# Kernel optimization log

Hardware: AMD Instinct MI355X
Metric: run time of the kernel (lower is better)

The kernel has to match this reference:

```python
import jax, jax.numpy as jnp
import numpy as np

# static configuration (matches init_kwargs)
CTX = 512   # context_dim
D = 512     # d_model
H = 8       # nhead
HD = D // H
L = 4       # num_layers
FF = 2048   # dim_feedforward
P = 24      # prediction_length
TS = 1      # time_series_dim
B = 256     # batch size
NEG = -1e9  # additive mask value (== -inf after softmax in fp32)


def _pos_encoding():
    pos = np.arange(P, dtype=np.float32)[:, None]
    div = np.exp(np.arange(0, D, 2, dtype=np.float32) * (-np.log(10000.0) / D))
    pe = np.zeros((P, D), dtype=np.float32)
    pe[:, 0::2] = np.sin(pos * div)
    pe[:, 1::2] = np.cos(pos * div)
    return jnp.asarray(pe[:, None, :])  # [P, 1, D] (seq-first broadcast over batch)


def setup_inputs() -> dict:
    key = jax.random.key(0)
    ks = iter(jax.random.split(key, 64))
    def g(shape, scale=0.02):
        return jax.random.normal(next(ks), shape, dtype=jnp.float32) * scale
    return {
        "context": jax.random.normal(next(ks), (B, CTX), dtype=jnp.float32),
        "start_token": g((1, 1, TS), 1.0),
        "ctx_W": g((D, CTX)), "ctx_b": jnp.zeros((D,), jnp.float32),
        "ve_W": g((D, TS)),   "ve_b": jnp.zeros((D,), jnp.float32),
        "sa_in_w": g((L, 3 * D, D)), "sa_in_b": jnp.zeros((L, 3 * D), jnp.float32),
        "sa_out_w": g((L, D, D)),    "sa_out_b": jnp.zeros((L, D), jnp.float32),
        "ca_in_w": g((L, 3 * D, D)), "ca_in_b": jnp.zeros((L, 3 * D), jnp.float32),
        "ca_out_w": g((L, D, D)),    "ca_out_b": jnp.zeros((L, D), jnp.float32),
        "lin1_w": g((L, FF, D)), "lin1_b": jnp.zeros((L, FF), jnp.float32),
        "lin2_w": g((L, D, FF)), "lin2_b": jnp.zeros((L, D), jnp.float32),
        "ln1_w": jnp.ones((L, D), jnp.float32), "ln1_b": jnp.zeros((L, D), jnp.float32),
        "ln2_w": jnp.ones((L, D), jnp.float32), "ln2_b": jnp.zeros((L, D), jnp.float32),
        "ln3_w": jnp.ones((L, D), jnp.float32), "ln3_b": jnp.zeros((L, D), jnp.float32),
        "o1_w": g((D // 2, D)), "o1_b": jnp.zeros((D // 2,), jnp.float32),
        "o2_w": g((TS, D // 2)), "o2_b": jnp.zeros((TS,), jnp.float32),
    }


def _layer_norm(x, w, b, eps=1e-5):
    m = jnp.mean(x, -1, keepdims=True)
    v = jnp.mean(jnp.square(x - m), -1, keepdims=True)
    return (x - m) / jnp.sqrt(v + eps) * w + b


def _mha(q_in, kv_in, in_w, in_b, out_w, out_b, mask):
    # q_in: [S,B,D] seq-first, kv_in: [T,B,D]
    Wq, Wk, Wv = jnp.split(in_w, 3, axis=0)
    bq, bk, bv = jnp.split(in_b, 3)
    S = q_in.shape[0]; T = kv_in.shape[0]
    q = (q_in @ Wq.T + bq).reshape(S, -1, H, HD)
    k = (kv_in @ Wk.T + bk).reshape(T, -1, H, HD)
    v = (kv_in @ Wv.T + bv).reshape(T, -1, H, HD)
    scores = jnp.einsum('sbhd,tbhd->bhst', q, k) / np.sqrt(HD).astype(np.float32)
    if mask is not None:
        scores = scores + mask
    attn = jax.nn.softmax(scores, axis=-1)
    o = jnp.einsum('bhst,tbhd->sbhd', attn, v).reshape(S, -1, D)
    return o @ out_w.T + out_b


def reference(context, start_token, ctx_W, ctx_b, ve_W, ve_b,
              sa_in_w, sa_in_b, sa_out_w, sa_out_b,
              ca_in_w, ca_in_b, ca_out_w, ca_out_b,
              lin1_w, lin1_b, lin2_w, lin2_b,
              ln1_w, ln1_b, ln2_w, ln2_b, ln3_w, ln3_b,
              o1_w, o1_b, o2_w, o2_b):
    pe = _pos_encoding()
    causal = jnp.where(jnp.tril(jnp.ones((P, P), bool)), 0.0, NEG)[None, None]  # [1,1,P,P]
    memory = (context @ ctx_W.T + ctx_b)[None]  # [1,B,D]

    def decode(vals):
        # vals: [P+1,B,TS]; only the first P slots form the (padded) target sequence.
        # Causal mask guarantees position t only sees slots <= t, so reading
        # position t reproduces the original length-(t+1) decode exactly.
        x = vals[:P] @ ve_W.T + ve_b + pe  # [P,B,D]
        for i in range(L):
            sa = _mha(x, x, sa_in_w[i], sa_in_b[i], sa_out_w[i], sa_out_b[i], causal)
            x = _layer_norm(x + sa, ln1_w[i], ln1_b[i])
            ca = _mha(x, memory, ca_in_w[i], ca_in_b[i], ca_out_w[i], ca_out_b[i], None)
            x = _layer_norm(x + ca, ln2_w[i], ln2_b[i])
            h = jax.nn.gelu(x @ lin1_w[i].T + lin1_b[i], approximate=False)
            x = _layer_norm(x + h @ lin2_w[i].T + lin2_b[i], ln3_w[i], ln3_b[i])
        return x

    def step(vals, t):
        x = decode(vals)
        last = jnp.take(x, t, axis=0)  # [B,D] output at current last position
        h = jax.nn.gelu(last @ o1_w.T + o1_b, approximate=False)
        nv = h @ o2_w.T + o2_b  # [B,TS]
        vals = jax.lax.dynamic_update_slice(vals, nv[None], (t + 1, 0, 0))
        return vals, nv

    vals0 = jnp.zeros((P + 1, B, TS), jnp.float32)
    vals0 = vals0.at[0].set(jnp.broadcast_to(start_token[0, 0], (B, TS)))
    _, ys = jax.lax.scan(jax.checkpoint(step), vals0, jnp.arange(P))
    return jnp.transpose(ys, (1, 0, 2))  # [B,P,TS]
```

## Files before the change

kernel.cpp:

```cpp
#include <hip/hip_runtime.h>
#include <math.h>


#define B    256
#define D    512
#define H    8
#define HD   64
#define L    4
#define FF   2048
#define P    24
#define NBLK 256
#define NTHR 512
#define NGRP 8
#define GSZ  32
#define CS   ((size_t)B * H * P * HD)

typedef float f4 __attribute__((ext_vector_type(4)));
typedef float f2 __attribute__((ext_vector_type(2)));

struct MegaArgs {
  const float *context, *start_token, *ctx_W, *ctx_b, *ve_W, *ve_b;
  const float *sa_in_w, *sa_in_b, *sa_out_w, *sa_out_b;
  const float *ca_in_w, *ca_in_b, *ca_out_w, *ca_out_b;
  const float *lin1_w, *lin1_b, *lin2_w, *lin2_b;
  const float *ln1_w, *ln1_b, *ln2_w, *ln2_b, *ln3_w, *ln3_b;
  const float *o1_w, *o1_b, *o2_w, *o2_b;
  float *out;
  float *pe, *vals, *memory, *ca_add, *x, *qbuf, *hbuf, *part, *hh,
        *kcache, *vcache;
};

__device__ __forceinline__ float gld(const float* p)
{
  return __hip_atomic_load((float*)p, __ATOMIC_RELAXED,
                           __HIP_MEMORY_SCOPE_AGENT);
}
__device__ __forceinline__ void gst(float* p, float v)
{
  __hip_atomic_store(p, v, __ATOMIC_RELAXED, __HIP_MEMORY_SCOPE_AGENT);
}
__device__ __forceinline__ void gst4(float* p, f4 v)
{
  asm volatile("global_store_dwordx4 %0, %1, off sc0 sc1"
               :: "v"(p), "v"(v) : "memory");
}
__device__ __forceinline__ f4 gld4e(const float* p)
{
  f4 r;
  asm volatile("global_load_dwordx4 %0, %1, off sc0 sc1\n\t"
               "s_waitcnt vmcnt(0)"
               : "=&v"(r) : "v"(p) : "memory");
  return r;
}

__device__ __align__(128) unsigned g_cnt[NGRP * 32];
__device__ __align__(128) unsigned g_root = 0;
__device__ __align__(128) unsigned g_gen  = 0;
__device__ __align__(128) unsigned g_base = 0;

__device__ __forceinline__ void grid_bar(unsigned &bno)
{
  ++bno;
  asm volatile("s_waitcnt vmcnt(0)" ::: "memory");
  __syncthreads();
  if (threadIdx.x == 0) {
    unsigned* cnt = &g_cnt[(blockIdx.x & (NGRP - 1)) * 32];
    const unsigned o = __hip_atomic_fetch_add(cnt, 1u, __ATOMIC_RELAXED,
                                              __HIP_MEMORY_SCOPE_AGENT);
    if (o == bno * GSZ - 1u) {
      const unsigned r = __hip_atomic_fetch_add(&g_root, 1u, __ATOMIC_RELAXED,
                                                __HIP_MEMORY_SCOPE_AGENT);
      if (r == bno * NGRP - 1u)
        __hip_atomic_store(&g_gen, bno, __ATOMIC_RELAXED,
                           __HIP_MEMORY_SCOPE_AGENT);
    }
    while (__hip_atomic_load(&g_gen, __ATOMIC_RELAXED,
                             __HIP_MEMORY_SCOPE_AGENT) < bno)
      __builtin_amdgcn_s_sleep(2);
  }
  __syncthreads();
}

__device__ __forceinline__ float gelu_f(float v)
{
  return 0.5f * v * (1.0f + erff(v * 0.70710678118654752f));
}
__device__ __forceinline__ f4 gelu4(f4 v)
{
  v.x = gelu_f(v.x); v.y = gelu_f(v.y); v.z = gelu_f(v.z); v.w = gelu_f(v.w);
  return v;
}

template <int LOADER, int EPI>
__device__ void gemmK(float* sh,
                      const float* A, int lda,
                      const float* W, int ldw, const float* bias,
                      float* C, int ldc, int m0, int n0, int k0, int KL,
                      float* kcp, float* vcp, int t,
                      const float* valst, const float* veW, const float* veb,
                      const float* pet)
{
  float* As = sh;
  float* Ws = sh + 16 * 68;
  const int tid = threadIdx.x;
  const int tm = tid >> 4;
  const int tn = tid & 15;
  float acc[2][4] = {};

  float vv0 = 0.f, vv1 = 0.f;
  if constexpr (LOADER == 1) {
    vv0 = valst[m0 + (tid >> 4)];
    vv1 = valst[m0 + 32 + (tid >> 4)];
  }

  for (int kb = 0; kb < KL; kb += 16) {
#pragma unroll
    for (int i = 0; i < 2; i++) {
      const int idx = tid + i * 512;
      const int r = idx >> 4;
      const int c = idx & 15;
      const int k = k0 + kb + c;
      float av;
      if constexpr (LOADER == 1) {
        av = (i ? vv1 : vv0) * veW[k] + veb[k] + pet[k];
      } else if constexpr (LOADER == 2) {
        av = A[(size_t)(m0 + r) * lda + k];
      } else {
        av = gld(A + (size_t)(m0 + r) * lda + k);
      }
      As[c * 68 + r] = av;
      Ws[c * 68 + r] = W[(size_t)(n0 + r) * ldw + k];
    }
    __syncthreads();
#pragma unroll
    for (int kk = 0; kk < 16; kk++) {
      const f2 a2 = *(const f2*)(As + kk * 68 + tm * 2);
      const f4 w4 = *(const f4*)(Ws + kk * 68 + tn * 4);
      acc[0][0] = fmaf(a2.x, w4.x, acc[0][0]);
      acc[0][1] = fmaf(a2.x, w4.y, acc[0][1]);
      acc[0][2] = fmaf(a2.x, w4.z, acc[0][2]);
      acc[0][3] = fmaf(a2.x, w4.w, acc[0][3]);
      acc[1][0] = fmaf(a2.y, w4.x, acc[1][0]);
      acc[1][1] = fmaf(a2.y, w4.y, acc[1][1]);
      acc[1][2] = fmaf(a2.y, w4.z, acc[1][2]);
      acc[1][3] = fmaf(a2.y, w4.w, acc[1][3]);
    }
    __syncthreads();
  }

  const int n4 = n0 + tn * 4;
#pragma unroll
  for (int i = 0; i < 2; i++) {
    const int m = m0 + tm * 2 + i;
    f4 v;
    v.x = acc[i][0]; v.y = acc[i][1]; v.z = acc[i][2]; v.w = acc[i][3];
    if constexpr (EPI != 3) v += *(const f4*)(bias + n4);
    if constexpr (EPI == 1) v = gelu4(v);
    if constexpr (EPI == 2) {
      if (n4 < D) {
        gst4(C + (size_t)m * D + n4, v);
      } else if (n4 < 2 * D) {
        const int f = n4 - D;
        gst4(kcp + ((size_t)(m * H + (f >> 6)) * P + t) * HD + (f & 63), v);
      } else {
        const int f = n4 - 2 * D;
        gst4(vcp + ((size_t)(m * H + (f >> 6)) * P + t) * HD + (f & 63), v);
      }
    } else {
      gst4(C + (size_t)m * ldc + n4, v);
    }
  }
}

__device__ __forceinline__ float rsum128(float v, float* sb)
{
#pragma unroll
  for (int o = 32; o; o >>= 1) v += __shfl_xor(v, o);
  const int w = threadIdx.x >> 6;
  if ((threadIdx.x & 63) == 0) sb[w] = v;
  __syncthreads();
  const int rl = threadIdx.x >> 7;
  const float s = sb[rl * 2] + sb[rl * 2 + 1];
  __syncthreads();
  return s;
}

#define NKMAP(b) ((((b) >> 5) << 3) | ((b) & 7))
#define MMAP(b)  (((b) >> 3) & 3)

__global__ __launch_bounds__(NTHR) void mega(MegaArgs a)
{
  __shared__ float sh[2 * 16 * 68];
  __shared__ float sbf[8];
  const int blk = blockIdx.x;
  unsigned bno = __hip_atomic_load(&g_base, __ATOMIC_RELAXED,
                                   __HIP_MEMORY_SCOPE_AGENT);
  float* attn_o = a.part + (size_t)4 * B * D;

  if (blk < 32) {
    gemmK<2, 0>(sh, a.context, 512, a.ctx_W, 512, a.ctx_b, a.memory, D,
                (blk & 3) * 64, (blk >> 2) * 64, 0, 512,
                nullptr, nullptr, 0, nullptr, nullptr, nullptr, nullptr);
  } else if (blk < 56) {
    const int tt = blk - 32;
    const int dd = threadIdx.x;
    const float fr = expf((float)(dd & ~1) * (-9.210340371976184f / (float)D));
    const float ang = (float)tt * fr;
    gst(a.pe + tt * D + dd, (dd & 1) ? cosf(ang) : sinf(ang));
  } else if (blk == 56) {
    if (threadIdx.x < B) gst(a.vals + threadIdx.x, a.start_token[0]);
  }
  grid_bar(bno);

  if (blk < 128) {
    const int l = blk >> 5, tile = blk & 31;
    gemmK<2, 0>(sh, a.memory, D,
                a.ca_in_w + (size_t)l * 3 * D * D + (size_t)2 * D * D, D,
                a.ca_in_b + l * 3 * D + 2 * D,
                a.part + (size_t)l * B * D, D,
                (tile & 3) * 64, (tile >> 2) * 64, 0, 512,
                nullptr, nullptr, 0, nullptr, nullptr, nullptr, nullptr);
  }
  grid_bar(bno);

  if (blk < 128) {
    const int l = blk >> 5, tile = blk & 31;
    gemmK<2, 0>(sh, a.part + (size_t)l * B * D, D,
                a.ca_out_w + (size_t)l * D * D, D, a.ca_out_b + l * D,
                a.ca_add + (size_t)l * B * D, D,
                (tile & 3) * 64, (tile >> 2) * 64, 0, 512,
                nullptr, nullptr, 0, nullptr, nullptr, nullptr, nullptr);
  }
  grid_bar(bno);

  for (int t = 0; t < P; t++) {
    for (int l = 0; l < L; l++) {
      float* kcp = a.kcache + (size_t)l * CS;
      float* vcp = a.vcache + (size_t)l * CS;

      if (blk < 96) {
        const int m0 = MMAP(blk) * 64, n0 = NKMAP(blk) * 64;
        if (l == 0)
          gemmK<1, 2>(sh, nullptr, 0, a.sa_in_w, D, a.sa_in_b, a.qbuf, D,
                      m0, n0, 0, 512, kcp, vcp, t,
                      a.vals + (size_t)t * B, a.ve_W, a.ve_b,
                      a.pe + (size_t)t * D);
        else
          gemmK<0, 2>(sh, a.x, D, a.sa_in_w + (size_t)l * 3 * D * D, D,
                      a.sa_in_b + l * 3 * D, a.qbuf, D, m0, n0, 0, 512,
                      kcp, vcp, t, nullptr, nullptr, nullptr, nullptr);
      }
      grid_bar(bno);

      {
        const int wid = threadIdx.x >> 6, lane = threadIdx.x & 63;
        const int u = blk * 8 + wid;
        const int b = u >> 3, h = u & 7;
        const int g = lane >> 4;
        const int hd0 = (lane & 15) * 4;
        const float* kb = kcp + (size_t)(b * H + h) * P * HD;
        const float* vb = vcp + (size_t)(b * H + h) * P * HD;
        const f4 q4 = gld4e(a.qbuf + (size_t)b * D + h * HD + hd0);
        const int nn = t + 1;
        float p[6];
#pragma unroll
        for (int bt = 0; bt < 6; bt++) {
          const int j = bt * 4 + g;
          float s = -1e30f;
          if (j < nn) {
            const f4 k4 = *(const f4*)(kb + j * HD + hd0);
            s = q4.x * k4.x + q4.y * k4.y + q4.z * k4.z + q4.w * k4.w;
          }
#pragma unroll
          for (int o = 1; o <= 8; o <<= 1) s += __shfl_xor(s, o);
          p[bt] = s * 0.125f;
        }
        float mx = -1e30f;
#pragma unroll
        for (int bt = 0; bt < 6; bt++)
          if (bt * 4 + g < nn) mx = fmaxf(mx, p[bt]);
        mx = fmaxf(mx, __shfl_xor(mx, 16));
        mx = fmaxf(mx, __shfl_xor(mx, 32));
        float sum = 0.f;
#pragma unroll
        for (int bt = 0; bt < 6; bt++) {
          const int j = bt * 4 + g;
          const float e = (j < nn) ? expf(p[bt] - mx) : 0.f;
          p[bt] = e; sum += e;
        }
        sum += __shfl_xor(sum, 16);
        sum += __shfl_xor(sum, 32);
        const float inv = 1.0f / sum;
        f4 o4 = {0.f, 0.f, 0.f, 0.f};
#pragma unroll
        for (int j = 0; j < P; j++)
          if (j < nn) {
            const float pj = __shfl(p[j >> 2], ((j & 3) << 4) | (lane & 15));
            const f4 v4 = *(const f4*)(vb + j * HD + hd0);
            o4 += (pj * inv) * v4;
          }
        gst4(attn_o + (size_t)b * D + h * HD + hd0, o4);
      }
      grid_bar(bno);

      if (blk < 128) {
        const int nk = NKMAP(blk);
        gemmK<0, 3>(sh, attn_o, D, a.sa_out_w + (size_t)l * D * D, D,
                    nullptr, a.part + (size_t)(nk >> 3) * B * D, D,
                    MMAP(blk) * 64, (nk & 7) * 64, (nk >> 3) * 128, 128,
                    nullptr, nullptr, 0, nullptr, nullptr, nullptr, nullptr);
      }
      grid_bar(bno);

      if (blk < 64) {
        const int row = blk * 4 + (threadIdx.x >> 7);
        const int cc = (threadIdx.x & 127) * 4;
        const size_t o = (size_t)row * D + cc;
        f4 u;
        if (l == 0) {
          const float vv = a.vals[(size_t)t * B + row];
          u = vv * (*(const f4*)(a.ve_W + cc)) + *(const f4*)(a.ve_b + cc)
              + *(const f4*)(a.pe + (size_t)t * D + cc);
        } else {
          u = gld4e(a.x + o);
        }
        u += *(const f4*)(a.sa_out_b + l * D + cc);
        u += gld4e(a.part + o);
        u += gld4e(a.part + (size_t)B * D + o);
        u += gld4e(a.part + (size_t)2 * B * D + o);
        u += gld4e(a.part + (size_t)3 * B * D + o);
        const float m1 = rsum128(u.x + u.y + u.z + u.w, sbf) * (1.0f / D);
        f4 d = u - m1;
        const float v1 =
            rsum128(d.x * d.x + d.y * d.y + d.z * d.z + d.w * d.w, sbf)
            * (1.0f / D);
        f4 z = d * rsqrtf(v1 + 1e-5f) * (*(const f4*)(a.ln1_w + l * D + cc))
               + *(const f4*)(a.ln1_b + l * D + cc);
        f4 r2 = z + *(const f4*)(a.ca_add + (size_t)l * B * D + o);
        const float m2 = rsum128(r2.x + r2.y + r2.z + r2.w, sbf) * (1.0f / D);
        f4 d2 = r2 - m2;
        const float v2 =
            rsum128(d2.x * d2.x + d2.y * d2.y + d2.z * d2.z + d2.w * d2.w,
                    sbf) * (1.0f / D);
        f4 z2 = d2 * rsqrtf(v2 + 1e-5f) * (*(const f4*)(a.ln2_w + l * D + cc))
                + *(const f4*)(a.ln2_b + l * D + cc);
        gst4(a.x + o, z2);
      }
      grid_bar(bno);

      if (blk < 128)
        gemmK<0, 1>(sh, a.x, D, a.lin1_w + (size_t)l * FF * D, D,
                    a.lin1_b + l * FF, a.hbuf, FF,
                    MMAP(blk) * 64, NKMAP(blk) * 64, 0, 512,
                    nullptr, nullptr, 0, nullptr, nullptr, nullptr, nullptr);
      grid_bar(bno);

      {
        const int nk = NKMAP(blk);
        gemmK<0, 3>(sh, a.hbuf, FF, a.lin2_w + (size_t)l * D * FF, FF,
                    nullptr, a.part + (size_t)(nk >> 3) * B * D, D,
                    MMAP(blk) * 64, (nk & 7) * 64, (nk >> 3) * 256, 256,
                    nullptr, nullptr, 0, nullptr, nullptr, nullptr, nullptr);
      }
      grid_bar(bno);

      if (blk < 64) {
        const int row = blk * 4 + (threadIdx.x >> 7);
        const int cc = (threadIdx.x & 127) * 4;
        const size_t o = (size_t)row * D + cc;
        f4 s0 = gld4e(a.x + o) + *(const f4*)(a.lin2_b + l * D + cc);
#pragma unroll
        for (int kc = 0; kc < 8; kc++)
          s0 += gld4e(a.part + (size_t)kc * B * D + o);
        const float m1 = rsum128(s0.x + s0.y + s0.z + s0.w, sbf) * (1.0f / D);
        f4 d = s0 - m1;
        const float v1 =
            rsum128(d.x * d.x + d.y * d.y + d.z * d.z + d.w * d.w, sbf)
            * (1.0f / D);
        f4 z = d * rsqrtf(v1 + 1e-5f) * (*(const f4*)(a.ln3_w + l * D + cc))
               + *(const f4*)(a.ln3_b + l * D + cc);
        gst4(a.x + o, z);
      }
      grid_bar(bno);
    }

    if (blk < 16)
      gemmK<0, 1>(sh, a.x, D, a.o1_w, D, a.o1_b, a.hh, 256,
                  (blk & 3) * 64, (blk >> 2) * 64, 0, 512,
                  nullptr, nullptr, 0, nullptr, nullptr, nullptr, nullptr);
    grid_bar(bno);

    if (blk < 32) {
      const int wid = threadIdx.x >> 6, lane = threadIdx.x & 63;
      const int r = blk * 8 + wid;
      const f4 hv = gld4e(a.hh + (size_t)r * 256 + lane * 4);
      const f4 wv = *(const f4*)(a.o2_w + lane * 4);
      float pp = hv.x * wv.x + hv.y * wv.y + hv.z * wv.z + hv.w * wv.w;
#pragma unroll
      for (int o = 32; o; o >>= 1) pp += __shfl_xor(pp, o);
      if (lane == 0) {
        const float v = pp + a.o2_b[0];
        gst(a.vals + (size_t)(t + 1) * B + r, v);
        a.out[(size_t)r * P + t] = v;
      }
    }
    grid_bar(bno);
  }

  if (blk == 0 && threadIdx.x == 0)
    __hip_atomic_store(&g_base, bno, __ATOMIC_RELAXED,
                       __HIP_MEMORY_SCOPE_AGENT);
}

extern "C" void kernel_launch(void* const* d_in, const int* in_sizes, int n_in,
                              void* d_out, int out_size, void* d_ws,
                              size_t ws_size, hipStream_t stream)
{
  (void)in_sizes; (void)n_in; (void)out_size; (void)ws_size;
  MegaArgs h;
  h.context     = (const float*)d_in[0];
  h.start_token = (const float*)d_in[1];
  h.ctx_W  = (const float*)d_in[2];
  h.ctx_b  = (const float*)d_in[3];
  h.ve_W   = (const float*)d_in[4];
  h.ve_b   = (const float*)d_in[5];
  h.sa_in_w  = (const float*)d_in[6];
  h.sa_in_b  = (const float*)d_in[7];
  h.sa_out_w = (const float*)d_in[8];
  h.sa_out_b = (const float*)d_in[9];
  h.ca_in_w  = (const float*)d_in[10];
  h.ca_in_b  = (const float*)d_in[11];
  h.ca_out_w = (const float*)d_in[12];
  h.ca_out_b = (const float*)d_in[13];
  h.lin1_w = (const float*)d_in[14];
  h.lin1_b = (const float*)d_in[15];
  h.lin2_w = (const float*)d_in[16];
  h.lin2_b = (const float*)d_in[17];
  h.ln1_w = (const float*)d_in[18];
  h.ln1_b = (const float*)d_in[19];
  h.ln2_w = (const float*)d_in[20];
  h.ln2_b = (const float*)d_in[21];
  h.ln3_w = (const float*)d_in[22];
  h.ln3_b = (const float*)d_in[23];
  h.o1_w = (const float*)d_in[24];
  h.o1_b = (const float*)d_in[25];
  h.o2_w = (const float*)d_in[26];
  h.o2_b = (const float*)d_in[27];
  h.out = (float*)d_out;

  float* ws = (float*)d_ws;
  size_t off = 0;
  h.pe      = ws + off; off += (size_t)P * D;
  h.vals    = ws + off; off += (size_t)(P + 1) * B;
  h.memory  = ws + off; off += (size_t)B * D;
  h.ca_add  = ws + off; off += (size_t)L * B * D;
  h.x       = ws + off; off += (size_t)B * D;
  h.qbuf    = ws + off; off += (size_t)B * D;
  h.hbuf    = ws + off; off += (size_t)B * FF;
  h.part    = ws + off; off += (size_t)8 * B * D;
  h.hh      = ws + off; off += (size_t)B * 256;
  h.kcache  = ws + off; off += (size_t)L * CS;
  h.vcache  = ws + off; off += (size_t)L * CS;

  void* kargs[] = { &h };
  hipLaunchCooperativeKernel(mega, dim3(NBLK), dim3(NTHR), kargs, 0, stream);
}
```

Before: 12.78 ms.

## Fuse per-row attention, out-proj and layernorms into one stage; double-buffer GEMM tiles

Restructures the decoder step so each block owns one batch row. That block scatters K/V into the cache, runs attention, does the self-attention output projection and the LN1/cross-attn/LN2 work in-block, and also runs the o1/o2 head. This removes several grid barriers per layer. The QKV GEMM now uses split-K over 192 blocks with the bias added during the fused stage. The shared GEMM is double-buffered with a 32-wide K chunk and prefetches the next tile, and the grid barrier spins on per-group generation flags. The trade-off is redundant per-row weight reads (sa_out_w, o1_w read by every block) in exchange for fewer synchronizations.

```diff
diff --git a/kernel.cpp b/kernel.cpp
--- a/kernel.cpp
+++ b/kernel.cpp
@@ -3,6 +3,7 @@
 
 
 #define B    256
+#define CTX  512
 #define D    512
 #define H    8
 #define HD   64
@@ -26,8 +27,7 @@
   const float *ln1_w, *ln1_b, *ln2_w, *ln2_b, *ln3_w, *ln3_b;
   const float *o1_w, *o1_b, *o2_w, *o2_b;
   float *out;
-  float *pe, *vals, *memory, *ca_add, *x, *qbuf, *hbuf, *part, *hh,
-        *kcache, *vcache;
+  float *pe, *vals, *ca_add, *x, *part, *hbuf, *kcache, *vcache;
 };
 
 __device__ __forceinline__ float gld(const float* p)
@@ -39,6 +39,17 @@
 {
   __hip_atomic_store(p, v, __ATOMIC_RELAXED, __HIP_MEMORY_SCOPE_AGENT);
 }
+#define GLD4(dst, ptr) \
+  asm volatile("global_load_dwordx4 %0, %1, off sc0 sc1" \
+               : "=&v"(dst) : "v"(ptr))
+#define GLD1(dst, ptr) \
+  asm volatile("global_load_dword %0, %1, off sc0 sc1" \
+               : "=&v"(dst) : "v"(ptr))
+__device__ __forceinline__ void gwait()
+{
+  asm volatile("s_waitcnt vmcnt(0)" ::: "memory");
+  __builtin_amdgcn_sched_barrier(0);
+}
 __device__ __forceinline__ void gst4(float* p, f4 v)
 {
   asm volatile("global_store_dwordx4 %0, %1, off sc0 sc1"
@@ -47,15 +58,14 @@
 __device__ __forceinline__ f4 gld4e(const float* p)
 {
   f4 r;
-  asm volatile("global_load_dwordx4 %0, %1, off sc0 sc1\n\t"
-               "s_waitcnt vmcnt(0)"
-               : "=&v"(r) : "v"(p) : "memory");
+  GLD4(r, p);
+  gwait();
   return r;
 }
 
 __device__ __align__(128) unsigned g_cnt[NGRP * 32];
 __device__ __align__(128) unsigned g_root = 0;
-__device__ __align__(128) unsigned g_gen  = 0;
+__device__ __align__(128) unsigned g_gen[NGRP * 32];
 __device__ __align__(128) unsigned g_base = 0;
 
 __device__ __forceinline__ void grid_bar(unsigned &bno)
@@ -64,19 +74,25 @@
   asm volatile("s_waitcnt vmcnt(0)" ::: "memory");
   __syncthreads();
   if (threadIdx.x == 0) {
-    unsigned* cnt = &g_cnt[(blockIdx.x & (NGRP - 1)) * 32];
-    const unsigned o = __hip_atomic_fetch_add(cnt, 1u, __ATOMIC_RELAXED,
-                                              __HIP_MEMORY_SCOPE_AGENT);
+    const int grp = blockIdx.x & (NGRP - 1);
+    const unsigned o = __hip_atomic_fetch_add(&g_cnt[grp * 32], 1u,
+                         __ATOMIC_RELAXED, __HIP_MEMORY_SCOPE_AGENT);
     if (o == bno * GSZ - 1u) {
-      const unsigned r = __hip_atomic_fetch_add(&g_root, 1u, __ATOMIC_RELAXED,
-                                                __HIP_MEMORY_SCOPE_AGENT);
-      if (r == bno * NGRP - 1u)
-        __hip_atomic_store(&g_gen, bno, __ATOMIC_RELAXED,
-                           __HIP_MEMORY_SCOPE_AGENT);
+      const unsigned r = __hip_atomic_fetch_add(&g_root, 1u,
+                           __ATOMIC_RELAXED, __HIP_MEMORY_SCOPE_AGENT);
+      if (r == bno * NGRP - 1u) {
+#pragma unroll
+        for (int g = 0; g < NGRP; g++)
+          __hip_atomic_store(&g_gen[g * 32], bno, __ATOMIC_RELAXED,
+                             __HIP_MEMORY_SCOPE_AGENT);
+      }
     }
-    while (__hip_atomic_load(&g_gen, __ATOMIC_RELAXED,
-                             __HIP_MEMORY_SCOPE_AGENT) < bno)
-      __builtin_amdgcn_s_sleep(2);
+    if (__hip_atomic_load(&g_gen[grp * 32], __ATOMIC_RELAXED,
+                          __HIP_MEMORY_SCOPE_AGENT) < bno) {
+      do { __builtin_amdgcn_s_sleep(16); }
+      while (__hip_atomic_load(&g_gen[grp * 32], __ATOMIC_RELAXED,
+                               __HIP_MEMORY_SCOPE_AGENT) < bno);
+    }
   }
   __syncthreads();
 }
@@ -92,50 +108,57 @@
 }
 
 template <int LOADER, int EPI>
-__device__ void gemmK(float* sh,
+__device__ void gemmK(float* shmem,
                       const float* A, int lda,
                       const float* W, int ldw, const float* bias,
                       float* C, int ldc, int m0, int n0, int k0, int KL,
-                      float* kcp, float* vcp, int t,
                       const float* valst, const float* veW, const float* veb,
                       const float* pet)
 {
-  float* As = sh;
-  float* Ws = sh + 16 * 68;
   const int tid = threadIdx.x;
+  const int r  = tid >> 3;
+  const int kl = (tid & 7) * 4;
   const int tm = tid >> 4;
   const int tn = tid & 15;
+
+  float vsc = 0.f;
+  if constexpr (LOADER == 1) vsc = valst[m0 + r];
+
+  f4 va, vw;
+  auto issue = [&](int kb) {
+    const int k = k0 + kb + kl;
+    if constexpr (LOADER == 1) {
+      va = vsc * (*(const f4*)(veW + k)) + (*(const f4*)(veb + k))
+           + (*(const f4*)(pet + k));
+    } else if constexpr (LOADER == 2) {
+      va = *(const f4*)(A + (size_t)(m0 + r) * lda + k);
+    } else {
+      GLD4(va, A + (size_t)(m0 + r) * lda + k);
+    }
+    vw = *(const f4*)(W + (size_t)(n0 + r) * ldw + k);
+  };
+
+  issue(0);
   float acc[2][4] = {};
-
-  float vv0 = 0.f, vv1 = 0.f;
-  if constexpr (LOADER == 1) {
-    vv0 = valst[m0 + (tid >> 4)];
-    vv1 = valst[m0 + 32 + (tid >> 4)];
-  }
-
-  for (int kb = 0; kb < KL; kb += 16) {
-#pragma unroll
-    for (int i = 0; i < 2; i++) {
-      const int idx = tid + i * 512;
-      const int r = idx >> 4;
-      const int c = idx & 15;
-      const int k = k0 + kb + c;
-      float av;
-      if constexpr (LOADER == 1) {
-        av = (i ? vv1 : vv0) * veW[k] + veb[k] + pet[k];
-      } else if constexpr (LOADER == 2) {
-        av = A[(size_t)(m0 + r) * lda + k];
-      } else {
-        av = gld(A + (size_t)(m0 + r) * lda + k);
-      }
-      As[c * 68 + r] = av;
-      Ws[c * 68 + r] = W[(size_t)(n0 + r) * ldw + k];
-    }
+  const int nch = KL / 32;
+  for (int ch = 0; ch < nch; ch++) {
+    float* as = shmem + (ch & 1) * (2 * 32 * 68);
+    float* ws = as + 32 * 68;
+    if constexpr (LOADER == 0) gwait();
+    as[(kl + 0) * 68 + r] = va.x;
+    as[(kl + 1) * 68 + r] = va.y;
+    as[(kl + 2) * 68 + r] = va.z;
+    as[(kl + 3) * 68 + r] = va.w;
+    ws[(kl + 0) * 68 + r] = vw.x;
+    ws[(kl + 1) * 68 + r] = vw.y;
+    ws[(kl + 2) * 68 + r] = vw.z;
+    ws[(kl + 3) * 68 + r] = vw.w;
     __syncthreads();
-#pragma unroll
-    for (int kk = 0; kk < 16; kk++) {
-      const f2 a2 = *(const f2*)(As + kk * 68 + tm * 2);
-      const f4 w4 = *(const f4*)(Ws + kk * 68 + tn * 4);
+    if (ch + 1 < nch) issue((ch + 1) * 32);
+#pragma unroll
+    for (int kk = 0; kk < 32; kk++) {
+      const f2 a2 = *(const f2*)(as + kk * 68 + tm * 2);
+      const f4 w4 = *(const f4*)(ws + kk * 68 + tn * 4);
       acc[0][0] = fmaf(a2.x, w4.x, acc[0][0]);
       acc[0][1] = fmaf(a2.x, w4.y, acc[0][1]);
       acc[0][2] = fmaf(a2.x, w4.z, acc[0][2]);
@@ -152,84 +175,74 @@
 #pragma unroll
   for (int i = 0; i < 2; i++) {
     const int m = m0 + tm * 2 + i;
-    f4 v;
-    v.x = acc[i][0]; v.y = acc[i][1]; v.z = acc[i][2]; v.w = acc[i][3];
+    f4 v = {acc[i][0], acc[i][1], acc[i][2], acc[i][3]};
     if constexpr (EPI != 3) v += *(const f4*)(bias + n4);
     if constexpr (EPI == 1) v = gelu4(v);
-    if constexpr (EPI == 2) {
-      if (n4 < D) {
-        gst4(C + (size_t)m * D + n4, v);
-      } else if (n4 < 2 * D) {
-        const int f = n4 - D;
-        gst4(kcp + ((size_t)(m * H + (f >> 6)) * P + t) * HD + (f & 63), v);
-      } else {
-        const int f = n4 - 2 * D;
-        gst4(vcp + ((size_t)(m * H + (f >> 6)) * P + t) * HD + (f & 63), v);
-      }
-    } else {
-      gst4(C + (size_t)m * ldc + n4, v);
-    }
-  }
-}
-
-__device__ __forceinline__ float rsum128(float v, float* sb)
+    gst4(C + (size_t)m * ldc + n4, v);
+  }
+}
+
+__device__ __forceinline__ float rsum512(float v, float* sbf)
 {
 #pragma unroll
   for (int o = 32; o; o >>= 1) v += __shfl_xor(v, o);
-  const int w = threadIdx.x >> 6;
-  if ((threadIdx.x & 63) == 0) sb[w] = v;
+  const int wid = threadIdx.x >> 6;
+  if ((threadIdx.x & 63) == 0) sbf[wid] = v;
   __syncthreads();
-  const int rl = threadIdx.x >> 7;
-  const float s = sb[rl * 2] + sb[rl * 2 + 1];
+  float s = 0.f;
+#pragma unroll
+  for (int w = 0; w < 8; w++) s += sbf[w];
   __syncthreads();
   return s;
 }
 
-#define NKMAP(b) ((((b) >> 5) << 3) | ((b) & 7))
-#define MMAP(b)  (((b) >> 3) & 3)
-
 __global__ __launch_bounds__(NTHR) void mega(MegaArgs a)
 {
-  __shared__ float sh[2 * 16 * 68];
+  __shared__ float sh[4 * 32 * 68];
+  __shared__ float rowbuf[1536];
+  __shared__ float attn_s[512];
   __shared__ float sbf[8];
   const int blk = blockIdx.x;
+  const int tid = threadIdx.x;
   unsigned bno = __hip_atomic_load(&g_base, __ATOMIC_RELAXED,
                                    __HIP_MEMORY_SCOPE_AGENT);
-  float* attn_o = a.part + (size_t)4 * B * D;
+
+  float* qkvA = a.part;
+  float* qkvB = a.part + (size_t)B * 1536;
+  float* memory = a.hbuf;
 
   if (blk < 32) {
-    gemmK<2, 0>(sh, a.context, 512, a.ctx_W, 512, a.ctx_b, a.memory, D,
+    gemmK<2, 0>(sh, a.context, CTX, a.ctx_W, CTX, a.ctx_b, memory, D,
                 (blk & 3) * 64, (blk >> 2) * 64, 0, 512,
-                nullptr, nullptr, 0, nullptr, nullptr, nullptr, nullptr);
+                nullptr, nullptr, nullptr, nullptr);
   } else if (blk < 56) {
     const int tt = blk - 32;
-    const int dd = threadIdx.x;
-    const float fr = expf((float)(dd & ~1) * (-9.210340371976184f / (float)D));
+    const float fr = expf((float)(tid & ~1) * (-9.210340371976184f / (float)D));
     const float ang = (float)tt * fr;
-    gst(a.pe + tt * D + dd, (dd & 1) ? cosf(ang) : sinf(ang));
+    gst(a.pe + tt * D + tid, (tid & 1) ? cosf(ang) : sinf(ang));
   } else if (blk == 56) {
-    if (threadIdx.x < B) gst(a.vals + threadIdx.x, a.start_token[0]);
+    if (tid < B) gst(a.vals + tid, a.start_token[0]);
   }
   grid_bar(bno);
 
   if (blk < 128) {
     const int l = blk >> 5, tile = blk & 31;
-    gemmK<2, 0>(sh, a.memory, D,
+    gemmK<0, 0>(sh, memory, D,
                 a.ca_in_w + (size_t)l * 3 * D * D + (size_t)2 * D * D, D,
                 a.ca_in_b + l * 3 * D + 2 * D,
                 a.part + (size_t)l * B * D, D,
                 (tile & 3) * 64, (tile >> 2) * 64, 0, 512,
-                nullptr, nullptr, 0, nullptr, nullptr, nullptr, nullptr);
+                nullptr, nullptr, nullptr, nullptr);
   }
   grid_bar(bno);
 
   if (blk < 128) {
     const int l = blk >> 5, tile = blk & 31;
-    gemmK<2, 0>(sh, a.part + (size_t)l * B * D, D,
+    gemmK<0, 0>(sh, a.part + (size_t)l * B * D, D,
                 a.ca_out_w + (size_t)l * D * D, D, a.ca_out_b + l * D,
                 a.ca_add + (size_t)l * B * D, D,
                 (tile & 3) * 64, (tile >> 2) * 64, 0, 512,
-                nullptr, nullptr, 0, nullptr, nullptr, nullptr, nullptr);
+                nullptr, nullptr, nullptr, nullptr);
   }
   grid_bar(bno);
 
@@ -238,176 +251,238 @@
       float* kcp = a.kcache + (size_t)l * CS;
       float* vcp = a.vcache + (size_t)l * CS;
 
-      if (blk < 96) {
-        const int m0 = MMAP(blk) * 64, n0 = NKMAP(blk) * 64;
+      if (blk < 192) {
+        const int wq = (blk >> 5) * 8 + (blk & 7);
+        const int m = (blk >> 3) & 3;
+        const int nt = wq >> 1, kc = wq & 1;
+        float* dst = kc ? qkvB : qkvA;
         if (l == 0)
-          gemmK<1, 2>(sh, nullptr, 0, a.sa_in_w, D, a.sa_in_b, a.qbuf, D,
-                      m0, n0, 0, 512, kcp, vcp, t,
+          gemmK<1, 3>(sh, nullptr, 0, a.sa_in_w, D, nullptr,
+                      dst, 1536, m * 64, nt * 64, kc * 256, 256,
                       a.vals + (size_t)t * B, a.ve_W, a.ve_b,
                       a.pe + (size_t)t * D);
         else
-          gemmK<0, 2>(sh, a.x, D, a.sa_in_w + (size_t)l * 3 * D * D, D,
-                      a.sa_in_b + l * 3 * D, a.qbuf, D, m0, n0, 0, 512,
-                      kcp, vcp, t, nullptr, nullptr, nullptr, nullptr);
+          gemmK<0, 3>(sh, a.x, D, a.sa_in_w + (size_t)l * 3 * D * D, D,
+                      nullptr, dst, 1536, m * 64, nt * 64, kc * 256, 256,
+                      nullptr, nullptr, nullptr, nullptr);
       }
       grid_bar(bno);
 
       {
-        const int wid = threadIdx.x >> 6, lane = threadIdx.x & 63;
-        const int u = blk * 8 + wid;
-        const int b = u >> 3, h = u & 7;
-        const int g = lane >> 4;
-        const int hd0 = (lane & 15) * 4;
-        const float* kb = kcp + (size_t)(b * H + h) * P * HD;
-        const float* vb = vcp + (size_t)(b * H + h) * P * HD;
-        const f4 q4 = gld4e(a.qbuf + (size_t)b * D + h * HD + hd0);
-        const int nn = t + 1;
-        float p[6];
-#pragma unroll
-        for (int bt = 0; bt < 6; bt++) {
-          const int j = bt * 4 + g;
-          float s = -1e30f;
-          if (j < nn) {
-            const f4 k4 = *(const f4*)(kb + j * HD + hd0);
-            s = q4.x * k4.x + q4.y * k4.y + q4.z * k4.z + q4.w * k4.w;
+        const int b = blk;
+        if (tid < 384) {
+          f4 pa, pb;
+          GLD4(pa, qkvA + (size_t)b * 1536 + tid * 4);
+          GLD4(pb, qkvB + (size_t)b * 1536 + tid * 4);
+          gwait();
+          f4 s = pa + pb + *(const f4*)(a.sa_in_b + l * 3 * D + tid * 4);
+          *(f4*)(rowbuf + tid * 4) = s;
+        }
+        __syncthreads();
+        if (tid < 256) {
+          const int half = tid >> 7;
+          const int d = (tid & 127) * 4;
+          const int h = d >> 6, hd = d & 63;
+          f4 kv = *(const f4*)(rowbuf + 512 + half * 512 + d);
+          float* cp = (half ? vcp : kcp)
+                      + ((size_t)(b * H + h) * P + t) * HD + hd;
+          gst4(cp, kv);
+        }
+        __syncthreads();
+        {
+          const int h = tid >> 6, lane = tid & 63;
+          const int g = lane >> 4, hd0 = (lane & 15) * 4;
+          const float* kb = kcp + (size_t)(b * H + h) * P * HD;
+          const float* vb = vcp + (size_t)(b * H + h) * P * HD;
+          const f4 q4 = *(const f4*)(rowbuf + h * HD + hd0);
+          const int nn = t + 1;
+          float pp[6];
+#pragma unroll
+          for (int bt = 0; bt < 6; bt++) {
+            const int j = bt * 4 + g;
+            float s = -1e30f;
+            if (j < nn) {
+              const f4 k4 = *(const f4*)(kb + j * HD + hd0);
+              s = q4.x * k4.x + q4.y * k4.y + q4.z * k4.z + q4.w * k4.w;
+            }
+#pragma unroll
+            for (int o = 1; o <= 8; o <<= 1) s += __shfl_xor(s, o);
+            pp[bt] = s * 0.125f;
           }
-#pragma unroll
-          for (int o = 1; o <= 8; o <<= 1) s += __shfl_xor(s, o);
-          p[bt] = s * 0.125f;
+          float mx = -1e30f;
+#pragma unroll
+          for (int bt = 0; bt < 6; bt++)
+            if (bt * 4 + g < nn) mx = fmaxf(mx, pp[bt]);
+          mx = fmaxf(mx, __shfl_xor(mx, 16));
+          mx = fmaxf(mx, __shfl_xor(mx, 32));
+          float sum = 0.f;
+#pragma unroll
+          for (int bt = 0; bt < 6; bt++) {
+            const int j = bt * 4 + g;
+            const float e = (j < nn) ? expf(pp[bt] - mx) : 0.f;
+            pp[bt] = e; sum += e;
+          }
+          sum += __shfl_xor(sum, 16);
+          sum += __shfl_xor(sum, 32);
+          const float inv = 1.0f / sum;
+          f4 o4 = {0.f, 0.f, 0.f, 0.f};
+#pragma unroll
+          for (int j = 0; j < P; j++)
+            if (j < nn) {
+              const float pj = __shfl(pp[j >> 2], ((j & 3) << 4) | (lane & 15));
+              const f4 v4 = *(const f4*)(vb + j * HD + hd0);
+              o4 += pj * v4;
+            }
+          o4 *= inv;
+          *(f4*)(attn_s + h * HD + hd0) = o4;
         }
-        float mx = -1e30f;
-#pragma unroll
-        for (int bt = 0; bt < 6; bt++)
-          if (bt * 4 + g < nn) mx = fmaxf(mx, p[bt]);
-        mx = fmaxf(mx, __shfl_xor(mx, 16));
-        mx = fmaxf(mx, __shfl_xor(mx, 32));
-        float sum = 0.f;
-#pragma unroll
-        for (int bt = 0; bt < 6; bt++) {
-          const int j = bt * 4 + g;
-          const float e = (j < nn) ? expf(p[bt] - mx) : 0.f;
-          p[bt] = e; sum += e;
+        __syncthreads();
+        {
+          const int n = tid;
+          const float* wrow = a.sa_out_w + (size_t)l * D * D + (size_t)n * D;
+          float xres;
+          if (l == 0) {
+            const float vv = a.vals[(size_t)t * B + b];
+            xres = vv * a.ve_W[n] + a.ve_b[n] + a.pe[(size_t)t * D + n];
+          } else {
+            xres = gld(a.x + (size_t)b * D + n);
+          }
+          float ac0 = 0.f, ac1 = 0.f, ac2 = 0.f, ac3 = 0.f;
+#pragma unroll 4
+          for (int k = 0; k < D; k += 16) {
+            const f4 w0 = *(const f4*)(wrow + k);
+            const f4 w1 = *(const f4*)(wrow + k + 4);
+            const f4 w2 = *(const f4*)(wrow + k + 8);
+            const f4 w3 = *(const f4*)(wrow + k + 12);
+            const f4 x0 = *(const f4*)(attn_s + k);
+            const f4 x1 = *(const f4*)(attn_s + k + 4);
+            const f4 x2 = *(const f4*)(attn_s + k + 8);
+            const f4 x3 = *(const f4*)(attn_s + k + 12);
+            ac0 = fmaf(w0.x, x0.x, ac0); ac0 = fmaf(w0.y, x0.y, ac0);
+            ac0 = fmaf(w0.z, x0.z, ac0); ac0 = fmaf(w0.w, x0.w, ac0);
+            ac1 = fmaf(w1.x, x1.x, ac1); ac1 = fmaf(w1.y, x1.y, ac1);
+            ac1 = fmaf(w1.z, x1.z, ac1); ac1 = fmaf(w1.w, x1.w, ac1);
+            ac2 = fmaf(w2.x, x2.x, ac2); ac2 = fmaf(w2.y, x2.y, ac2);
+            ac2 = fmaf(w2.z, x2.z, ac2); ac2 = fmaf(w2.w, x2.w, ac2);
+            ac3 = fmaf(w3.x, x3.x, ac3); ac3 = fmaf(w3.y, x3.y, ac3);
+            ac3 = fmaf(w3.z, x3.z, ac3); ac3 = fmaf(w3.w, x3.w, ac3);
+          }
+          float u = xres + (ac0 + ac1) + (ac2 + ac3) + a.sa_out_b[l * D + n];
+          const float m1 = rsum512(u, sbf) * (1.0f / D);
+          const float d1 = u - m1;
+          const float v1 = rsum512(d1 * d1, sbf) * (1.0f / D);
+          float z = d1 * rsqrtf(v1 + 1e-5f) * a.ln1_w[l * D + n]
+                    + a.ln1_b[l * D + n];
+          z += a.ca_add[(size_t)l * B * D + (size_t)b * D + n];
+          const float m2 = rsum512(z, sbf) * (1.0f / D);
+          const float d2 = z - m2;
+          const float v2 = rsum512(d2 * d2, sbf) * (1.0f / D);
+          rowbuf[n] = d2 * rsqrtf(v2 + 1e-5f) * a.ln2_w[l * D + n]
+                      + a.ln2_b[l * D + n];
         }
-        sum += __shfl_xor(sum, 16);
-        sum += __shfl_xor(sum, 32);
-        const float inv = 1.0f / sum;
-        f4 o4 = {0.f, 0.f, 0.f, 0.f};
-#pragma unroll
-        for (int j = 0; j < P; j++)
-          if (j < nn) {
-            const float pj = __shfl(p[j >> 2], ((j & 3) << 4) | (lane & 15));
-            const f4 v4 = *(const f4*)(vb + j * HD + hd0);
-            o4 += (pj * inv) * v4;
-          }
-        gst4(attn_o + (size_t)b * D + h * HD + hd0, o4);
+        __syncthreads();
+        if (tid < 128)
+          gst4(a.x + (size_t)blk * D + tid * 4, *(const f4*)(rowbuf + tid * 4));
       }
       grid_bar(bno);
 
       if (blk < 128) {
-        const int nk = NKMAP(blk);
-        gemmK<0, 3>(sh, attn_o, D, a.sa_out_w + (size_t)l * D * D, D,
-                    nullptr, a.part + (size_t)(nk >> 3) * B * D, D,
-                    MMAP(blk) * 64, (nk & 7) * 64, (nk >> 3) * 128, 128,
-                    nullptr, nullptr, 0, nullptr, nullptr, nullptr, nullptr);
-      }
-      grid_bar(bno);
-
-      if (blk < 64) {
-        const int row = blk * 4 + (threadIdx.x >> 7);
-        const int cc = (threadIdx.x & 127) * 4;
-        const size_t o = (size_t)row * D + cc;
-        f4 u;
-        if (l == 0) {
-          const float vv = a.vals[(size_t)t * B + row];
-          u = vv * (*(const f4*)(a.ve_W + cc)) + *(const f4*)(a.ve_b + cc)
-              + *(const f4*)(a.pe + (size_t)t * D + cc);
-        } else {
-          u = gld4e(a.x + o);
-        }
-        u += *(const f4*)(a.sa_out_b + l * D + cc);
-        u += gld4e(a.part + o);
-        u += gld4e(a.part + (size_t)B * D + o);
-        u += gld4e(a.part + (size_t)2 * B * D + o);
-        u += gld4e(a.part + (size_t)3 * B * D + o);
-        const float m1 = rsum128(u.x + u.y + u.z + u.w, sbf) * (1.0f / D);
-        f4 d = u - m1;
-        const float v1 =
-            rsum128(d.x * d.x + d.y * d.y + d.z * d.z + d.w * d.w, sbf)
-            * (1.0f / D);
-        f4 z = d * rsqrtf(v1 + 1e-5f) * (*(const f4*)(a.ln1_w + l * D + cc))
-               + *(const f4*)(a.ln1_b + l * D + cc);
-        f4 r2 = z + *(const f4*)(a.ca_add + (size_t)l * B * D + o);
-        const float m2 = rsum128(r2.x + r2.y + r2.z + r2.w, sbf) * (1.0f / D);
-        f4 d2 = r2 - m2;
-        const float v2 =
-            rsum128(d2.x * d2.x + d2.y * d2.y + d2.z * d2.z + d2.w * d2.w,
-                    sbf) * (1.0f / D);
-        f4 z2 = d2 * rsqrtf(v2 + 1e-5f) * (*(const f4*)(a.ln2_w + l * D + cc))
-                + *(const f4*)(a.ln2_b + l * D + cc);
-        gst4(a.x + o, z2);
-      }
-      grid_bar(bno);
-
-      if (blk < 128)
+        const int wt = (blk >> 5) * 8 + (blk & 7);
+        const int m = (blk >> 3) & 3;
         gemmK<0, 1>(sh, a.x, D, a.lin1_w + (size_t)l * FF * D, D,
                     a.lin1_b + l * FF, a.hbuf, FF,
-                    MMAP(blk) * 64, NKMAP(blk) * 64, 0, 512,
-                    nullptr, nullptr, 0, nullptr, nullptr, nullptr, nullptr);
+                    m * 64, wt * 64, 0, 512,
+                    nullptr, nullptr, nullptr, nullptr);
+      }
       grid_bar(bno);
 
       {
-        const int nk = NKMAP(blk);
+        const int wt = (blk >> 5) * 8 + (blk & 7);
+        const int m = (blk >> 3) & 3;
+        const int nt = wt >> 3, kc = wt & 7;
         gemmK<0, 3>(sh, a.hbuf, FF, a.lin2_w + (size_t)l * D * FF, FF,
-                    nullptr, a.part + (size_t)(nk >> 3) * B * D, D,
-                    MMAP(blk) * 64, (nk & 7) * 64, (nk >> 3) * 256, 256,
-                    nullptr, nullptr, 0, nullptr, nullptr, nullptr, nullptr);
+                    nullptr, a.part + (size_t)kc * B * D, D,
+                    m * 64, nt * 64, kc * 256, 256,
+                    nullptr, nullptr, nullptr, nullptr);
       }
       grid_bar(bno);
 
-      if (blk < 64) {
-        const int row = blk * 4 + (threadIdx.x >> 7);
-        const int cc = (threadIdx.x & 127) * 4;
-        const size_t o = (size_t)row * D + cc;
-        f4 s0 = gld4e(a.x + o) + *(const f4*)(a.lin2_b + l * D + cc);
-#pragma unroll
-        for (int kc = 0; kc < 8; kc++)
-          s0 += gld4e(a.part + (size_t)kc * B * D + o);
-        const float m1 = rsum128(s0.x + s0.y + s0.z + s0.w, sbf) * (1.0f / D);
-        f4 d = s0 - m1;
-        const float v1 =
-            rsum128(d.x * d.x + d.y * d.y + d.z * d.z + d.w * d.w, sbf)
-            * (1.0f / D);
-        f4 z = d * rsqrtf(v1 + 1e-5f) * (*(const f4*)(a.ln3_w + l * D + cc))
-               + *(const f4*)(a.ln3_b + l * D + cc);
-        gst4(a.x + o, z);
+      {
+        const int b = blk, n = tid;
+        const size_t o = (size_t)b * D + n;
+        float xv, p0, p1, p2, p3, p4, p5, p6, p7;
+        GLD1(xv, a.x + o);
+        GLD1(p0, a.part + o);
+        GLD1(p1, a.part + (size_t)1 * B * D + o);
+        GLD1(p2, a.part + (size_t)2 * B * D + o);
+        GLD1(p3, a.part + (size_t)3 * B * D + o);
+        GLD1(p4, a.part + (size_t)4 * B * D + o);
+        GLD1(p5, a.part + (size_t)5 * B * D + o);
+        GLD1(p6, a.part + (size_t)6 * B * D + o);
+        GLD1(p7, a.part + (size_t)7 * B * D + o);
+        gwait();
+        float s0 = xv + a.lin2_b[l * D + n]
+                 + ((p0 + p1) + (p2 + p3)) + ((p4 + p5) + (p6 + p7));
+        const float m1 = rsum512(s0, sbf) * (1.0f / D);
+        const float d1 = s0 - m1;
+        const float v1 = rsum512(d1 * d1, sbf) * (1.0f / D);
+        rowbuf[n] = d1 * rsqrtf(v1 + 1e-5f) * a.ln3_w[l * D + n]
+                    + a.ln3_b[l * D + n];
+        __syncthreads();
+        if (tid < 128)
+          gst4(a.x + (size_t)b * D + tid * 4, *(const f4*)(rowbuf + tid * 4));
       }
       grid_bar(bno);
     }
 
-    if (blk < 16)
-      gemmK<0, 1>(sh, a.x, D, a.o1_w, D, a.o1_b, a.hh, 256,
-                  (blk & 3) * 64, (blk >> 2) * 64, 0, 512,
-                  nullptr, nullptr, 0, nullptr, nullptr, nullptr, nullptr);
-    grid_bar(bno);
-
-    if (blk < 32) {
-      const int wid = threadIdx.x >> 6, lane = threadIdx.x & 63;
-      const int r = blk * 8 + wid;
-      const f4 hv = gld4e(a.hh + (size_t)r * 256 + lane * 4);
-      const f4 wv = *(const f4*)(a.o2_w + lane * 4);
-      float pp = hv.x * wv.x + hv.y * wv.y + hv.z * wv.z + hv.w * wv.w;
-#pragma unroll
-      for (int o = 32; o; o >>= 1) pp += __shfl_xor(pp, o);
-      if (lane == 0) {
-        const float v = pp + a.o2_b[0];
-        gst(a.vals + (size_t)(t + 1) * B + r, v);
-        a.out[(size_t)r * P + t] = v;
+    {
+      const int b = blk;
+      if (tid < 128)
+        *(f4*)(rowbuf + tid * 4) = gld4e(a.x + (size_t)b * D + tid * 4);
+      __syncthreads();
+      if (tid < 256) {
+        const float* wrow = a.o1_w + (size_t)tid * D;
+        float ac0 = 0.f, ac1 = 0.f, ac2 = 0.f, ac3 = 0.f;
+#pragma unroll 4
+        for (int k = 0; k < D; k += 16) {
+          const f4 w0 = *(const f4*)(wrow + k);
+          const f4 w1 = *(const f4*)(wrow + k + 4);
+          const f4 w2 = *(const f4*)(wrow + k + 8);
+          const f4 w3 = *(const f4*)(wrow + k + 12);
+          const f4 x0 = *(const f4*)(rowbuf + k);
+          const f4 x1 = *(const f4*)(rowbuf + k + 4);
+          const f4 x2 = *(const f4*)(rowbuf + k + 8);
+          const f4 x3 = *(const f4*)(rowbuf + k + 12);
+          ac0 = fmaf(w0.x, x0.x, ac0); ac0 = fmaf(w0.y, x0.y, ac0);
+          ac0 = fmaf(w0.z, x0.z, ac0); ac0 = fmaf(w0.w, x0.w, ac0);
+          ac1 = fmaf(w1.x, x1.x, ac1); ac1 = fmaf(w1.y, x1.y, ac1);
+          ac1 = fmaf(w1.z, x1.z, ac1); ac1 = fmaf(w1.w, x1.w, ac1);
+          ac2 = fmaf(w2.x, x2.x, ac2); ac2 = fmaf(w2.y, x2.y, ac2);
+          ac2 = fmaf(w2.z, x2.z, ac2); ac2 = fmaf(w2.w, x2.w, ac2);
+          ac3 = fmaf(w3.x, x3.x, ac3); ac3 = fmaf(w3.y, x3.y, ac3);
+          ac3 = fmaf(w3.z, x3.z, ac3); ac3 = fmaf(w3.w, x3.w, ac3);
+        }
+        attn_s[tid] = gelu_f((ac0 + ac1) + (ac2 + ac3) + a.o1_b[tid]);
+      }
+      __syncthreads();
+      if (tid < 64) {
+        float p = 0.f;
+#pragma unroll
+        for (int j = 0; j < 4; j++)
+          p = fmaf(attn_s[tid * 4 + j], a.o2_w[tid * 4 + j], p);
+#pragma unroll
+        for (int o = 32; o; o >>= 1) p += __shfl_xor(p, o);
+        if (tid == 0) {
+          const float v = p + a.o2_b[0];
+          gst(a.vals + (size_t)(t + 1) * B + b, v);
+          a.out[(size_t)b * P + t] = v;
+        }
       }
     }
     grid_bar(bno);
   }
 
-  if (blk == 0 && threadIdx.x == 0)
+  if (blk == 0 && tid == 0)
     __hip_atomic_store(&g_base, bno, __ATOMIC_RELAXED,
                        __HIP_MEMORY_SCOPE_AGENT);
 }
@@ -452,13 +527,10 @@
   size_t off = 0;
   h.pe      = ws + off; off += (size_t)P * D;
   h.vals    = ws + off; off += (size_t)(P + 1) * B;
-  h.memory  = ws + off; off += (size_t)B * D;
   h.ca_add  = ws + off; off += (size_t)L * B * D;
   h.x       = ws + off; off += (size_t)B * D;
-  h.qbuf    = ws + off; off += (size_t)B * D;
+  h.part    = ws + off; off += (size_t)8 * B * D;
   h.hbuf    = ws + off; off += (size_t)B * FF;
-  h.part    = ws + off; off += (size_t)8 * B * D;
-  h.hh      = ws + off; off += (size_t)B * 256;
   h.kcache  = ws + off; off += (size_t)L * CS;
   h.vcache  = ws + off; off += (size_t)L * CS;
 
```

Result: faster. 11.08 ms (-13.3%).
